# Performance work log

Hardware: AMD Instinct MI355X
Metric: run time of the kernel (lower is better)

## Reference

```python
import jax, jax.numpy as jnp
import numpy as np
from jax import lax

J = 3  # number of decomposition levels
SQ2 = float(1.0 / np.sqrt(2.0))


def _corr(Xp, hr, axis, Lout, stride):
    """Strided valid correlation of padded Xp with taps hr along `axis`.
    out[n] = sum_k hr[k] * Xp[n*stride + k]. Tap loop is over <=10 static taps."""
    m = hr.shape[0]
    hi = stride * (Lout - 1) + 1
    acc = hr[0] * lax.slice_in_dim(Xp, 0, hi, stride, axis)
    for k in range(1, m):
        acc = acc + hr[k] * lax.slice_in_dim(Xp, k, k + hi, stride, axis)
    return acc


def colfilter(X, h):
    # 'same' convolution along H with symmetric (edge-repeat) extension.
    m = h.shape[0]; m2 = m // 2; L = X.shape[2]
    Xp = jnp.pad(X, ((0, 0), (0, 0), (m2, m2), (0, 0)), mode='symmetric')
    return _corr(Xp, h[::-1], 2, L, 1)  # corr with reversed taps == convolution


def rowfilter(X, h):
    m = h.shape[0]; m2 = m // 2; L = X.shape[3]
    Xp = jnp.pad(X, ((0, 0), (0, 0), (0, 0), (m2, m2)), mode='symmetric')
    return _corr(Xp, h[::-1], 3, L, 1)


def coldfilt(X, ha, hb, highpass):
    # Dual-tree decimated (by 2) filtering along H. r must be a multiple of 4.
    b, c, r, w = X.shape
    m = ha.shape[0]; r4 = r // 4
    Xp = jnp.pad(X, ((0, 0), (0, 0), (m, m), (0, 0)), mode='symmetric')
    E = Xp[:, :, 2::2, :]  # even-phase stream, len r/2+m-1
    O = Xp[:, :, 3::2, :]  # odd-phase stream
    a_out = _corr(O, ha[::-1], 2, r4, 2)
    b_out = _corr(E, hb[::-1], 2, r4, 2)
    ev, od = (b_out, a_out) if highpass else (a_out, b_out)
    return jnp.stack([ev, od], axis=3).reshape(b, c, r // 2, w)


def rowdfilt(X, ha, hb, highpass):
    b, c, r, w = X.shape
    m = ha.shape[0]; w4 = w // 4
    Xp = jnp.pad(X, ((0, 0), (0, 0), (0, 0), (m, m)), mode='symmetric')
    E = Xp[:, :, :, 2::2]
    O = Xp[:, :, :, 3::2]
    a_out = _corr(O, ha[::-1], 3, w4, 2)
    b_out = _corr(E, hb[::-1], 3, w4, 2)
    ev, od = (b_out, a_out) if highpass else (a_out, b_out)
    return jnp.stack([ev, od], axis=4).reshape(b, c, r, w // 2)


def q2c(y):
    # Convert quads of real pixels into two complex subbands.
    y = y * SQ2
    a = y[..., 0::2, 0::2]; b = y[..., 0::2, 1::2]
    c = y[..., 1::2, 0::2]; d = y[..., 1::2, 1::2]
    return (a - d, b + c), (a + d, b - c)


def _bands(lh, hh, hl):
    # Orientation order [15, 45, 75, 105, 135, 165] deg; real/imag in last dim.
    (r15, i15), (r165, i165) = q2c(lh)
    (r45, i45), (r135, i135) = q2c(hh)
    (r75, i75), (r105, i105) = q2c(hl)
    c = lambda re, im: jnp.stack([re, im], axis=-1)
    return jnp.stack([c(r15, i15), c(r45, i45), c(r75, i75),
                      c(r105, i105), c(r135, i135), c(r165, i165)], axis=2)


def dtcwt_forward(x, h0o, h1o, h0a, h0b, h1a, h1b):
    # Level 1 (undecimated biorthogonal filters; q2c decimates bandpass by 2).
    lo = rowfilter(x, h0o)
    hi = rowfilter(x, h1o)
    ll = colfilter(lo, h0o)
    yh = [_bands(colfilter(lo, h1o), colfilter(hi, h1o), colfilter(hi, h0o))]
    # Levels 2..J (quarter-shift dual-tree decimated filters).
    for _ in range(1, J):
        lo = rowdfilt(ll, h0b, h0a, False)
        hi = rowdfilt(ll, h1b, h1a, True)
        lh = coldfilt(lo, h1b, h1a, True)
        hl = coldfilt(hi, h0b, h0a, False)
        hh = coldfilt(hi, h1b, h1a, True)
        ll = coldfilt(lo, h0b, h0a, False)
        yh.append(_bands(lh, hh, hl))
    return (ll, yh[0], yh[1], yh[2])


def _filters():
    h0o = np.array([-0.05, 0.25, 0.6, 0.25, -0.05], dtype=np.float32)
    h1o = np.array([-3/280, 3/56, 73/280, -17/28, 73/280, 3/56, -3/280],
                   dtype=np.float32)
    h0a = np.array([0.03516384, 0.0, -0.08832942, 0.23389032, 0.76027237,
                    0.58751830, 0.0, -0.11430184, 0.0, 0.0], dtype=np.float32)
    h0b = h0a[::-1].copy()
    alt = ((-1.0) ** np.arange(10)).astype(np.float32)
    h1a = h0b * alt
    h1b = h1a[::-1].copy()
    return {k: jnp.asarray(v) for k, v in dict(
        h0o=h0o, h1o=h1o, h0a=h0a, h0b=h0b, h1a=h1a, h1b=h1b).items()}


def setup_inputs() -> dict:
    key = jax.random.key(0)
    x = jax.random.normal(key, (8, 16, 256, 256), dtype=jnp.float32)
    inp = {'x': x}
    inp.update(_filters())
    return inp


def reference(x, h0o, h1o, h0a, h0b, h1a, h1b):
    return dtcwt_forward(x, h0o, h1o, h0a, h0b, h1a, h1b)
```

## Files before the change

### kernel.cpp

```cpp
#include <hip/hip_runtime.h>

#define SQ2F 0.70710678118654752440f

static constexpr float H0O[5] = {-0.05f, 0.25f, 0.6f, 0.25f, -0.05f};
static constexpr float H1O[7] = {(float)(-3.0/280.0), (float)(3.0/56.0), (float)(73.0/280.0),
                                 (float)(-17.0/28.0), (float)(73.0/280.0), (float)(3.0/56.0),
                                 (float)(-3.0/280.0)};
static constexpr float H0A[10] = {0.03516384f, 0.0f, -0.08832942f, 0.23389032f, 0.76027237f,
                                  0.5875183f, 0.0f, -0.11430184f, 0.0f, 0.0f};
static constexpr float H0B[10] = {0.0f, 0.0f, -0.11430184f, 0.0f, 0.5875183f,
                                  0.76027237f, 0.23389032f, -0.08832942f, 0.0f, 0.03516384f};
static constexpr float H1A[10] = {0.0f, 0.0f, -0.11430184f, 0.0f, 0.5875183f,
                                  -0.76027237f, 0.23389032f, 0.08832942f, 0.0f, -0.03516384f};
static constexpr float H1B[10] = {-0.03516384f, 0.0f, 0.08832942f, 0.23389032f, -0.76027237f,
                                  0.5875183f, 0.0f, -0.11430184f, 0.0f, 0.0f};

__device__ __forceinline__ int symref(int t, int L) {
    if (t < 0) t = -1 - t;
    if (t >= L) t = 2 * L - 1 - t;
    return t;
}

#define XS(r,c)  S[(r)*85 + (c)]
#define LS(r,c)  S[(r)*81 + (c)]
#define LOS(r,c) S[4420 + (r)*81 + (c)]
#define LO2(r,c) S[4420 + (r)*33 + (c)]
#define HI2(r,c) S[6004 + (r)*33 + (c)]
#define HIS(r,c) S[8632 + (r)*71 + (c)]

__global__ __launch_bounds__(256) void dtcwt_l12(
    const float* __restrict__ x,
    float* __restrict__ yh0,
    float* __restrict__ yh1,
    float* __restrict__ ll2)
{
    __shared__ float S[11472];
    int tid = threadIdx.x, bx = blockIdx.x;
    int tj = bx & 3, ti = (bx >> 2) & 7, bc = bx >> 5;
    const int xr0 = 32 * ti - 10, xc0 = 64 * tj - 10;
    const float* xb = x + (size_t)bc * 65536;

    for (int p = tid; p < 52 * 84; p += 256) {
        int r = p / 84, c = p - r * 84;
        XS(r, c) = xb[symref(xr0 + r, 256) * 256 + symref(xc0 + c, 256)];
    }
    __syncthreads();

    for (int p = tid; p < 4160; p += 256) {
        int r = p % 52, c = p / 52;
        float l = 0.f;
        #pragma unroll
        for (int t = 0; t < 5; t++) l += H0O[t] * XS(r, c + 4 - t);
        LOS(r, c) = l;
    }
    for (int p = tid; p < 2800; p += 256) {
        int r = p % 40, c = p / 40;
        float h = 0.f;
        #pragma unroll
        for (int t = 0; t < 7; t++) h += H1O[t] * XS(7 + r, c + 10 - t);
        HIS(r, c) = h;
    }
    __syncthreads();

    for (int p = tid; p < 3840; p += 256) {
        int c = p % 80, r = p / 80;
        float v = 0.f;
        #pragma unroll
        for (int t = 0; t < 5; t++) v += H0O[t] * LOS(r + 4 - t, c);
        LS(r, c) = v;
    }
    {
        float* yb = yh0 + (size_t)bc * 196608;
        const size_t bs = 32768;
        for (int q = tid; q < 512; q += 256) {
            int oj = q & 31, oi = q >> 5;
            int i0 = 16 * ti + oi, j0 = 32 * tj + oj;
            float low[8][2], hiw[8][2];
            #pragma unroll
            for (int k = 0; k < 8; k++) {
                low[k][0] = LOS(2 * oi + 7 + k, 2 * oj + 8);
                low[k][1] = LOS(2 * oi + 7 + k, 2 * oj + 9);
                hiw[k][0] = HIS(2 * oi + k,     2 * oj + 3);
                hiw[k][1] = HIS(2 * oi + k,     2 * oj + 4);
            }
            float lh[2][2] = {}, hh[2][2] = {}, hl[2][2] = {};
            #pragma unroll
            for (int t = 0; t < 7; t++) {
                #pragma unroll
                for (int d = 0; d < 2; d++) {
                    lh[d][0] += H1O[t] * low[d + 6 - t][0];
                    lh[d][1] += H1O[t] * low[d + 6 - t][1];
                    hh[d][0] += H1O[t] * hiw[d + 6 - t][0];
                    hh[d][1] += H1O[t] * hiw[d + 6 - t][1];
                }
            }
            #pragma unroll
            for (int t = 0; t < 5; t++) {
                #pragma unroll
                for (int d = 0; d < 2; d++) {
                    hl[d][0] += H0O[t] * hiw[d + 5 - t][0];
                    hl[d][1] += H0O[t] * hiw[d + 5 - t][1];
                }
            }
            size_t pix = ((size_t)i0 * 128 + j0) * 2;
            {
                float a = SQ2F*lh[0][0], b = SQ2F*lh[0][1], c = SQ2F*lh[1][0], d = SQ2F*lh[1][1];
                *(float2*)&yb[0*bs + pix] = make_float2(a - d, b + c);
                *(float2*)&yb[5*bs + pix] = make_float2(a + d, b - c);
            }
            {
                float a = SQ2F*hh[0][0], b = SQ2F*hh[0][1], c = SQ2F*hh[1][0], d = SQ2F*hh[1][1];
                *(float2*)&yb[1*bs + pix] = make_float2(a - d, b + c);
                *(float2*)&yb[4*bs + pix] = make_float2(a + d, b - c);
            }
            {
                float a = SQ2F*hl[0][0], b = SQ2F*hl[0][1], c = SQ2F*hl[1][0], d = SQ2F*hl[1][1];
                *(float2*)&yb[2*bs + pix] = make_float2(a - d, b + c);
                *(float2*)&yb[3*bs + pix] = make_float2(a + d, b - c);
            }
        }
    }
    __syncthreads();

    for (int p = tid; p < 768; p += 256) {
        int r = p % 48, nl = p / 48;
        int gc = 64 * tj + 4 * nl - 8;
        float v[20];
        #pragma unroll
        for (int k = 0; k < 20; k++)
            v[k] = LS(r, symref(gc + k, 256) - 64 * tj + 8);
        float aLo = 0.f, bLo = 0.f, aHi = 0.f, bHi = 0.f;
        #pragma unroll
        for (int t = 0; t < 10; t++) {
            float vo = v[19 - 2 * t], ve = v[18 - 2 * t];
            aLo += H0B[t] * vo; bLo += H0A[t] * ve;
            aHi += H1B[t] * vo; bHi += H1A[t] * ve;
        }
        LO2(r, 2*nl)   = aLo;
        LO2(r, 2*nl+1) = bLo;
        HI2(r, 2*nl)   = bHi;
        HI2(r, 2*nl+1) = aHi;
    }
    __syncthreads();

    if (tid < 128) {
        int lj = tid & 15, li = tid >> 4;
        int i1 = 8 * ti + li, j1 = 16 * tj + lj;

        float ll_[2][2], lh_[2][2], hl_[2][2], hh_[2][2];
        #pragma unroll
        for (int cc = 0; cc < 2; cc++) {
            int c = 2 * lj + cc;
            float vl[20], vh[20];
            #pragma unroll
            for (int k = 0; k < 20; k++) {
                int loc = symref(32 * ti + 4 * li - 8 + k, 256) - 32 * ti + 8;
                vl[k] = LO2(loc, c);
                vh[k] = HI2(loc, c);
            }
            float a_ll=0,b_ll=0,a_lh=0,b_lh=0,a_hl=0,b_hl=0,a_hh=0,b_hh=0;
            #pragma unroll
            for (int t = 0; t < 10; t++) {
                float vo_l = vl[19 - 2*t], ve_l = vl[18 - 2*t];
                float vo_h = vh[19 - 2*t], ve_h = vh[18 - 2*t];
                a_ll += H0B[t] * vo_l;  b_ll += H0A[t] * ve_l;
                a_lh += H1B[t] * vo_l;  b_lh += H1A[t] * ve_l;
                a_hl += H0B[t] * vo_h;  b_hl += H0A[t] * ve_h;
                a_hh += H1B[t] * vo_h;  b_hh += H1A[t] * ve_h;
            }
            ll_[0][cc] = a_ll; ll_[1][cc] = b_ll;
            lh_[0][cc] = b_lh; lh_[1][cc] = a_lh;
            hl_[0][cc] = a_hl; hl_[1][cc] = b_hl;
            hh_[0][cc] = b_hh; hh_[1][cc] = a_hh;
        }

        float* llb = ll2 + (size_t)bc * 16384;
        *(float2*)&llb[(size_t)(2*i1)  *128 + 2*j1] = make_float2(ll_[0][0], ll_[0][1]);
        *(float2*)&llb[(size_t)(2*i1+1)*128 + 2*j1] = make_float2(ll_[1][0], ll_[1][1]);

        float* yb = yh1 + (size_t)bc * 49152;
        size_t pix = ((size_t)i1 * 64 + j1) * 2;
        const size_t bs = 8192;
        {
            float a = SQ2F*lh_[0][0], b = SQ2F*lh_[0][1], c = SQ2F*lh_[1][0], d = SQ2F*lh_[1][1];
            *(float2*)&yb[0*bs + pix] = make_float2(a - d, b + c);
            *(float2*)&yb[5*bs + pix] = make_float2(a + d, b - c);
        }
        {
            float a = SQ2F*hh_[0][0], b = SQ2F*hh_[0][1], c = SQ2F*hh_[1][0], d = SQ2F*hh_[1][1];
            *(float2*)&yb[1*bs + pix] = make_float2(a - d, b + c);
            *(float2*)&yb[4*bs + pix] = make_float2(a + d, b - c);
        }
        {
            float a = SQ2F*hl_[0][0], b = SQ2F*hl_[0][1], c = SQ2F*hl_[1][0], d = SQ2F*hl_[1][1];
            *(float2*)&yb[2*bs + pix] = make_float2(a - d, b + c);
            *(float2*)&yb[3*bs + pix] = make_float2(a + d, b - c);
        }
    }
}

__global__ __launch_bounds__(256) void level_fused(
    const float* __restrict__ X,
    float* __restrict__ llout,
    float* __restrict__ yh,
    int R, int C, int nbi, int nbj)
{
    __shared__ float Xs[80][81];
    __shared__ float Lo[80][33];
    __shared__ float Hi[80][33];

    int tid = threadIdx.x;
    int bx  = blockIdx.x;
    int tj = bx % nbj; int ti = (bx / nbj) % nbi; int bc = bx / (nbj * nbi);
    int i0 = ti * 16, j0 = tj * 16;
    int gr0 = 4 * i0 - 8, gc0 = 4 * j0 - 8;
    const float* Xb = X + (size_t)bc * R * C;

    for (int p = tid; p < 80 * 80; p += 256) {
        int r = p / 80, c = p - r * 80;
        Xs[r][c] = Xb[(size_t)symref(gr0 + r, R) * C + symref(gc0 + c, C)];
    }
    __syncthreads();

    for (int p = tid; p < 80 * 16; p += 256) {
        int nl = p / 80, r = p - nl * 80;
        float v[20];
        #pragma unroll
        for (int k = 0; k < 20; k++) v[k] = Xs[r][4 * nl + k];
        float aLo = 0.f, bLo = 0.f, aHi = 0.f, bHi = 0.f;
        #pragma unroll
        for (int t = 0; t < 10; t++) {
            float vo = v[19 - 2 * t], ve = v[18 - 2 * t];
            aLo += H0B[t] * vo; bLo += H0A[t] * ve;
            aHi += H1B[t] * vo; bHi += H1A[t] * ve;
        }
        Lo[r][2*nl]   = aLo;
        Lo[r][2*nl+1] = bLo;
        Hi[r][2*nl]   = bHi;
        Hi[r][2*nl+1] = aHi;
    }
    __syncthreads();

    int R4 = R >> 2, Wq = C >> 2, C2 = C >> 1;
    int lj = tid & 15, li = tid >> 4;
    int i = i0 + li, j = j0 + lj;

    float ll_[2][2], lh_[2][2], hl_[2][2], hh_[2][2];
    #pragma unroll
    for (int cc = 0; cc < 2; cc++) {
        int c = 2 * lj + cc;
        float vl[20], vh[20];
        #pragma unroll
        for (int k = 0; k < 20; k++) {
            vl[k] = Lo[4 * li + k][c];
            vh[k] = Hi[4 * li + k][c];
        }
        float a_ll=0,b_ll=0,a_lh=0,b_lh=0,a_hl=0,b_hl=0,a_hh=0,b_hh=0;
        #pragma unroll
        for (int t = 0; t < 10; t++) {
            float vo_l = vl[19 - 2*t], ve_l = vl[18 - 2*t];
            float vo_h = vh[19 - 2*t], ve_h = vh[18 - 2*t];
            a_ll += H0B[t] * vo_l;  b_ll += H0A[t] * ve_l;
            a_lh += H1B[t] * vo_l;  b_lh += H1A[t] * ve_l;
            a_hl += H0B[t] * vo_h;  b_hl += H0A[t] * ve_h;
            a_hh += H1B[t] * vo_h;  b_hh += H1A[t] * ve_h;
        }
        ll_[0][cc] = a_ll; ll_[1][cc] = b_ll;
        lh_[0][cc] = b_lh; lh_[1][cc] = a_lh;
        hl_[0][cc] = a_hl; hl_[1][cc] = b_hl;
        hh_[0][cc] = b_hh; hh_[1][cc] = a_hh;
    }

    float* llb = llout + (size_t)bc * (R >> 1) * C2;
    llb[(size_t)(2*i)*C2   + 2*j]     = ll_[0][0];
    llb[(size_t)(2*i)*C2   + 2*j + 1] = ll_[0][1];
    llb[(size_t)(2*i+1)*C2 + 2*j]     = ll_[1][0];
    llb[(size_t)(2*i+1)*C2 + 2*j + 1] = ll_[1][1];

    float* yb = yh + (size_t)bc * 6 * R4 * Wq * 2;
    size_t pix = ((size_t)i * Wq + j) * 2;
    size_t bs  = (size_t)R4 * Wq * 2;
    {
        float a = SQ2F*lh_[0][0], b = SQ2F*lh_[0][1], c = SQ2F*lh_[1][0], d = SQ2F*lh_[1][1];
        yb[0*bs + pix] = a - d; yb[0*bs + pix + 1] = b + c;
        yb[5*bs + pix] = a + d; yb[5*bs + pix + 1] = b - c;
    }
    {
        float a = SQ2F*hh_[0][0], b = SQ2F*hh_[0][1], c = SQ2F*hh_[1][0], d = SQ2F*hh_[1][1];
        yb[1*bs + pix] = a - d; yb[1*bs + pix + 1] = b + c;
        yb[4*bs + pix] = a + d; yb[4*bs + pix + 1] = b - c;
    }
    {
        float a = SQ2F*hl_[0][0], b = SQ2F*hl_[0][1], c = SQ2F*hl_[1][0], d = SQ2F*hl_[1][1];
        yb[2*bs + pix] = a - d; yb[2*bs + pix + 1] = b + c;
        yb[3*bs + pix] = a + d; yb[3*bs + pix + 1] = b - c;
    }
}

extern "C" void kernel_launch(void* const* d_in, const int* in_sizes, int n_in,
                              void* d_out, int out_size, void* d_ws, size_t ws_size,
                              hipStream_t stream) {
    const float* x = (const float*)d_in[0];
    float* out = (float*)d_out;

    const int BC = 8 * 16;

    float* out_ll  = out;
    float* out_yh0 = out + 524288;
    float* out_yh1 = out + 25690112;
    float* out_yh2 = out + 31981568;

    float* ll2 = (float*)d_ws;

    dtcwt_l12<<<BC * 32, 256, 0, stream>>>(x, out_yh0, out_yh1, ll2);

    level_fused<<<BC * 4, 256, 0, stream>>>(ll2, out_ll, out_yh2, 128, 128, 2, 2);
}
```

Measured before the change: 227.1 us.

## Double block size and give one output column per thread with shuffle-based q2c

Raises the level-1/2 fused kernel to 512 threads per block. The yh0 and yh1 output stages now compute one column per thread and use lane shuffles to form the q2c complex pairs, with even and odd lanes writing different subbands. This spreads the per-thread register load and serial work across more threads and raises parallelism in the tail stages. The cost is more threads idle in some phases (the tid<256 stage) and larger blocks, which may reduce how many blocks fit per CU.

```diff
diff --git a/kernel.cpp b/kernel.cpp
--- a/kernel.cpp
+++ b/kernel.cpp
@@ -28,7 +28,7 @@
 #define HI2(r,c) S[6004 + (r)*33 + (c)]
 #define HIS(r,c) S[8632 + (r)*71 + (c)]
 
-__global__ __launch_bounds__(256) void dtcwt_l12(
+__global__ __launch_bounds__(512) void dtcwt_l12(
     const float* __restrict__ x,
     float* __restrict__ yh0,
     float* __restrict__ yh1,
@@ -40,20 +40,20 @@
     const int xr0 = 32 * ti - 10, xc0 = 64 * tj - 10;
     const float* xb = x + (size_t)bc * 65536;
 
-    for (int p = tid; p < 52 * 84; p += 256) {
+    for (int p = tid; p < 52 * 84; p += 512) {
         int r = p / 84, c = p - r * 84;
         XS(r, c) = xb[symref(xr0 + r, 256) * 256 + symref(xc0 + c, 256)];
     }
     __syncthreads();
 
-    for (int p = tid; p < 4160; p += 256) {
+    for (int p = tid; p < 4160; p += 512) {
         int r = p % 52, c = p / 52;
         float l = 0.f;
         #pragma unroll
         for (int t = 0; t < 5; t++) l += H0O[t] * XS(r, c + 4 - t);
         LOS(r, c) = l;
     }
-    for (int p = tid; p < 2800; p += 256) {
+    for (int p = tid; p < 2800; p += 512) {
         int r = p % 40, c = p / 40;
         float h = 0.f;
         #pragma unroll
@@ -62,7 +62,7 @@
     }
     __syncthreads();
 
-    for (int p = tid; p < 3840; p += 256) {
+    for (int p = tid; p < 3840; p += 512) {
         int c = p % 80, r = p / 80;
         float v = 0.f;
         #pragma unroll
@@ -72,57 +72,46 @@
     {
         float* yb = yh0 + (size_t)bc * 196608;
         const size_t bs = 32768;
-        for (int q = tid; q < 512; q += 256) {
-            int oj = q & 31, oi = q >> 5;
-            int i0 = 16 * ti + oi, j0 = 32 * tj + oj;
-            float low[8][2], hiw[8][2];
+        int lane = tid & 63;
+        #pragma unroll
+        for (int it = 0; it < 2; ++it) {
+            int oi = (tid >> 6) + 8 * it;
+            float low[8], hiw[8];
             #pragma unroll
             for (int k = 0; k < 8; k++) {
-                low[k][0] = LOS(2 * oi + 7 + k, 2 * oj + 8);
-                low[k][1] = LOS(2 * oi + 7 + k, 2 * oj + 9);
-                hiw[k][0] = HIS(2 * oi + k,     2 * oj + 3);
-                hiw[k][1] = HIS(2 * oi + k,     2 * oj + 4);
-            }
-            float lh[2][2] = {}, hh[2][2] = {}, hl[2][2] = {};
+                low[k] = LOS(2 * oi + 7 + k, 8 + lane);
+                hiw[k] = HIS(2 * oi + k,     3 + lane);
+            }
+            float lh_e = 0, lh_o = 0, hh_e = 0, hh_o = 0, hl_e = 0, hl_o = 0;
             #pragma unroll
             for (int t = 0; t < 7; t++) {
-                #pragma unroll
-                for (int d = 0; d < 2; d++) {
-                    lh[d][0] += H1O[t] * low[d + 6 - t][0];
-                    lh[d][1] += H1O[t] * low[d + 6 - t][1];
-                    hh[d][0] += H1O[t] * hiw[d + 6 - t][0];
-                    hh[d][1] += H1O[t] * hiw[d + 6 - t][1];
-                }
+                lh_e += H1O[t] * low[6 - t]; lh_o += H1O[t] * low[7 - t];
+                hh_e += H1O[t] * hiw[6 - t]; hh_o += H1O[t] * hiw[7 - t];
             }
             #pragma unroll
             for (int t = 0; t < 5; t++) {
-                #pragma unroll
-                for (int d = 0; d < 2; d++) {
-                    hl[d][0] += H0O[t] * hiw[d + 5 - t][0];
-                    hl[d][1] += H0O[t] * hiw[d + 5 - t][1];
-                }
-            }
+                hl_e += H0O[t] * hiw[5 - t]; hl_o += H0O[t] * hiw[6 - t];
+            }
+            lh_e *= SQ2F; lh_o *= SQ2F; hh_e *= SQ2F; hh_o *= SQ2F; hl_e *= SQ2F; hl_o *= SQ2F;
+            float u_lh = lh_e - __shfl_xor(lh_o, 1), v_lh = __shfl_xor(lh_e, 1) + lh_o;
+            float u_hh = hh_e - __shfl_xor(hh_o, 1), v_hh = __shfl_xor(hh_e, 1) + hh_o;
+            float u_hl = hl_e - __shfl_xor(hl_o, 1), v_hl = __shfl_xor(hl_e, 1) + hl_o;
+            int i0 = 16 * ti + oi, j0 = 32 * tj + (lane >> 1);
             size_t pix = ((size_t)i0 * 128 + j0) * 2;
-            {
-                float a = SQ2F*lh[0][0], b = SQ2F*lh[0][1], c = SQ2F*lh[1][0], d = SQ2F*lh[1][1];
-                *(float2*)&yb[0*bs + pix] = make_float2(a - d, b + c);
-                *(float2*)&yb[5*bs + pix] = make_float2(a + d, b - c);
-            }
-            {
-                float a = SQ2F*hh[0][0], b = SQ2F*hh[0][1], c = SQ2F*hh[1][0], d = SQ2F*hh[1][1];
-                *(float2*)&yb[1*bs + pix] = make_float2(a - d, b + c);
-                *(float2*)&yb[4*bs + pix] = make_float2(a + d, b - c);
-            }
-            {
-                float a = SQ2F*hl[0][0], b = SQ2F*hl[0][1], c = SQ2F*hl[1][0], d = SQ2F*hl[1][1];
-                *(float2*)&yb[2*bs + pix] = make_float2(a - d, b + c);
-                *(float2*)&yb[3*bs + pix] = make_float2(a + d, b - c);
-            }
-        }
-    }
-    __syncthreads();
-
-    for (int p = tid; p < 768; p += 256) {
+            if ((lane & 1) == 0) {
+                *(float2*)&yb[0 * bs + pix] = make_float2(u_lh, v_lh);
+                *(float2*)&yb[1 * bs + pix] = make_float2(u_hh, v_hh);
+                *(float2*)&yb[2 * bs + pix] = make_float2(u_hl, v_hl);
+            } else {
+                *(float2*)&yb[5 * bs + pix] = make_float2(v_lh, u_lh);
+                *(float2*)&yb[4 * bs + pix] = make_float2(v_hh, u_hh);
+                *(float2*)&yb[3 * bs + pix] = make_float2(v_hl, u_hl);
+            }
+        }
+    }
+    __syncthreads();
+
+    for (int p = tid; p < 768; p += 512) {
         int r = p % 48, nl = p / 48;
         int gc = 64 * tj + 4 * nl - 8;
         float v[20];
@@ -143,58 +132,49 @@
     }
     __syncthreads();
 
-    if (tid < 128) {
-        int lj = tid & 15, li = tid >> 4;
-        int i1 = 8 * ti + li, j1 = 16 * tj + lj;
-
-        float ll_[2][2], lh_[2][2], hl_[2][2], hh_[2][2];
-        #pragma unroll
-        for (int cc = 0; cc < 2; cc++) {
-            int c = 2 * lj + cc;
-            float vl[20], vh[20];
-            #pragma unroll
-            for (int k = 0; k < 20; k++) {
-                int loc = symref(32 * ti + 4 * li - 8 + k, 256) - 32 * ti + 8;
-                vl[k] = LO2(loc, c);
-                vh[k] = HI2(loc, c);
-            }
-            float a_ll=0,b_ll=0,a_lh=0,b_lh=0,a_hl=0,b_hl=0,a_hh=0,b_hh=0;
-            #pragma unroll
-            for (int t = 0; t < 10; t++) {
-                float vo_l = vl[19 - 2*t], ve_l = vl[18 - 2*t];
-                float vo_h = vh[19 - 2*t], ve_h = vh[18 - 2*t];
-                a_ll += H0B[t] * vo_l;  b_ll += H0A[t] * ve_l;
-                a_lh += H1B[t] * vo_l;  b_lh += H1A[t] * ve_l;
-                a_hl += H0B[t] * vo_h;  b_hl += H0A[t] * ve_h;
-                a_hh += H1B[t] * vo_h;  b_hh += H1A[t] * ve_h;
-            }
-            ll_[0][cc] = a_ll; ll_[1][cc] = b_ll;
-            lh_[0][cc] = b_lh; lh_[1][cc] = a_lh;
-            hl_[0][cc] = a_hl; hl_[1][cc] = b_hl;
-            hh_[0][cc] = b_hh; hh_[1][cc] = a_hh;
-        }
-
+    if (tid < 256) {
+        int c  = tid & 31;
+        int li = tid >> 5;
+        int i1 = 8 * ti + li;
+        float vl[20], vh[20];
+        #pragma unroll
+        for (int k = 0; k < 20; k++) {
+            int loc = symref(32 * ti + 4 * li - 8 + k, 256) - 32 * ti + 8;
+            vl[k] = LO2(loc, c);
+            vh[k] = HI2(loc, c);
+        }
+        float a_ll=0,b_ll=0,a_lh=0,b_lh=0,a_hl=0,b_hl=0,a_hh=0,b_hh=0;
+        #pragma unroll
+        for (int t = 0; t < 10; t++) {
+            float vo_l = vl[19 - 2*t], ve_l = vl[18 - 2*t];
+            float vo_h = vh[19 - 2*t], ve_h = vh[18 - 2*t];
+            a_ll += H0B[t] * vo_l;  b_ll += H0A[t] * ve_l;
+            a_lh += H1B[t] * vo_l;  b_lh += H1A[t] * ve_l;
+            a_hl += H0B[t] * vo_h;  b_hl += H0A[t] * ve_h;
+            a_hh += H1B[t] * vo_h;  b_hh += H1A[t] * ve_h;
+        }
         float* llb = ll2 + (size_t)bc * 16384;
-        *(float2*)&llb[(size_t)(2*i1)  *128 + 2*j1] = make_float2(ll_[0][0], ll_[0][1]);
-        *(float2*)&llb[(size_t)(2*i1+1)*128 + 2*j1] = make_float2(ll_[1][0], ll_[1][1]);
-
+        int gcol = 32 * tj + c;
+        llb[(size_t)(2*i1)   * 128 + gcol] = a_ll;
+        llb[(size_t)(2*i1+1) * 128 + gcol] = b_ll;
+        float lh_e = SQ2F*b_lh, lh_o = SQ2F*a_lh;
+        float hh_e = SQ2F*b_hh, hh_o = SQ2F*a_hh;
+        float hl_e = SQ2F*a_hl, hl_o = SQ2F*b_hl;
+        float u_lh = lh_e - __shfl_xor(lh_o, 1), v_lh = __shfl_xor(lh_e, 1) + lh_o;
+        float u_hh = hh_e - __shfl_xor(hh_o, 1), v_hh = __shfl_xor(hh_e, 1) + hh_o;
+        float u_hl = hl_e - __shfl_xor(hl_o, 1), v_hl = __shfl_xor(hl_e, 1) + hl_o;
         float* yb = yh1 + (size_t)bc * 49152;
+        int j1 = 16 * tj + (c >> 1);
         size_t pix = ((size_t)i1 * 64 + j1) * 2;
         const size_t bs = 8192;
-        {
-            float a = SQ2F*lh_[0][0], b = SQ2F*lh_[0][1], c = SQ2F*lh_[1][0], d = SQ2F*lh_[1][1];
-            *(float2*)&yb[0*bs + pix] = make_float2(a - d, b + c);
-            *(float2*)&yb[5*bs + pix] = make_float2(a + d, b - c);
-        }
-        {
-            float a = SQ2F*hh_[0][0], b = SQ2F*hh_[0][1], c = SQ2F*hh_[1][0], d = SQ2F*hh_[1][1];
-            *(float2*)&yb[1*bs + pix] = make_float2(a - d, b + c);
-            *(float2*)&yb[4*bs + pix] = make_float2(a + d, b - c);
-        }
-        {
-            float a = SQ2F*hl_[0][0], b = SQ2F*hl_[0][1], c = SQ2F*hl_[1][0], d = SQ2F*hl_[1][1];
-            *(float2*)&yb[2*bs + pix] = make_float2(a - d, b + c);
-            *(float2*)&yb[3*bs + pix] = make_float2(a + d, b - c);
+        if ((c & 1) == 0) {
+            *(float2*)&yb[0 * bs + pix] = make_float2(u_lh, v_lh);
+            *(float2*)&yb[1 * bs + pix] = make_float2(u_hh, v_hh);
+            *(float2*)&yb[2 * bs + pix] = make_float2(u_hl, v_hl);
+        } else {
+            *(float2*)&yb[5 * bs + pix] = make_float2(v_lh, u_lh);
+            *(float2*)&yb[4 * bs + pix] = make_float2(v_hh, u_hh);
+            *(float2*)&yb[3 * bs + pix] = make_float2(v_hl, u_hl);
         }
     }
 }
@@ -312,7 +292,7 @@
 
     float* ll2 = (float*)d_ws;
 
-    dtcwt_l12<<<BC * 32, 256, 0, stream>>>(x, out_yh0, out_yh1, ll2);
+    dtcwt_l12<<<BC * 32, 512, 0, stream>>>(x, out_yh0, out_yh1, ll2);
 
     level_fused<<<BC * 4, 256, 0, stream>>>(ll2, out_ll, out_yh2, 128, 128, 2, 2);
 }
```

Result: no change. 229.0 us (+0.8%).
